# Optimization experiments

Hardware: AMD Instinct MI355X
Metric: run time of the kernel (lower is better)

Reference implementation:

```python
import jax, jax.numpy as jnp
import numpy as np

D, H, W = 64, 128, 128
NUM_LABELS = 2
NUM_ITERS = 5
SIGMA_SPATIAL_BLUR = 1.0   # sigma for the pure spatial Gaussian filter
BLUR_RADIUS = 2            # 5-tap separable kernel
SIGMA_BILAT_SPATIAL = 1.5  # spatial sigma of bilateral filter
SIGMA_BILAT_RANGE = 0.5    # intensity (range) sigma of bilateral filter
LOG_SQRT_2PI = 0.5 * float(np.log(2.0 * np.pi))


def _shift(x, axis, off):
    # zero-padded shift: out[i] = x[i - off] along `axis` (static off)
    if off == 0:
        return x
    pad = [(0, 0)] * x.ndim
    sl = [slice(None)] * x.ndim
    if off > 0:
        pad[axis] = (off, 0)
        sl[axis] = slice(0, x.shape[axis])
    else:
        pad[axis] = (0, -off)
        sl[axis] = slice(-off, x.shape[axis] - off)
    return jnp.pad(x, pad)[tuple(sl)]


def _shift3(x, dz, dy, dx):
    return _shift(_shift(_shift(x, 2, dz), 3, dy), 4, dx)


_offs = np.arange(-BLUR_RADIUS, BLUR_RADIUS + 1)
_k1d = np.exp(-_offs.astype(np.float64) ** 2 / (2.0 * SIGMA_SPATIAL_BLUR ** 2))
_k1d = (_k1d / _k1d.sum()).astype(np.float32)


def _gaussian_blur3d(x):
    # separable normalized Gaussian over the 3 spatial axes (zero padding)
    for ax in (2, 3, 4):
        x = sum(float(_k1d[i]) * _shift(x, ax, int(_offs[i])) for i in range(len(_offs)))
    return x


def _bilateral_weights(image):
    # precompute 27 neighbor weight maps (image is constant across CRF iterations)
    ws, offsets = [], []
    for dz in (-1, 0, 1):
        for dy in (-1, 0, 1):
            for dx in (-1, 0, 1):
                d2 = float(dz * dz + dy * dy + dx * dx)
                img_s = _shift3(image, dz, dy, dx)
                w = jnp.exp(-d2 / (2.0 * SIGMA_BILAT_SPATIAL ** 2)
                            - (image - img_s) ** 2 / (2.0 * SIGMA_BILAT_RANGE ** 2))
                ws.append(w)
                offsets.append((dz, dy, dx))
    den = sum(ws)  # (1,1,D,H,W), broadcasts over labels
    return ws, den, offsets


def _bilateral_apply(q, ws, den, offsets):
    num = sum(w * _shift3(q, dz, dy, dx) for w, (dz, dy, dx) in zip(ws, offsets))
    return num / den


def _crfrnn(image, logits, unary, spatial_w, bilateral_w, compat):
    ws, den, offsets = _bilateral_weights(image)
    cur = logits
    for _ in range(NUM_ITERS):
        qs = jax.nn.softmax(cur, axis=1)                      # (1,L,D,H,W)
        sp = _gaussian_blur3d(qs)                             # spatial message
        bl = _bilateral_apply(qs, ws, den, offsets)           # bilateral message
        msg = (jnp.einsum('lm,bmdhw->bldhw', spatial_w, sp)
               + jnp.einsum('lm,bmdhw->bldhw', bilateral_w, bl))
        pairwise = jnp.einsum('lm,bmdhw->bldhw', compat, msg)
        cur = unary - pairwise
    return jax.nn.softmax(cur, axis=1)


def setup_inputs() -> dict:
    key = jax.random.key(0)
    k1, k2, k3, k4, k5, k6 = jax.random.split(key, 6)
    image = jax.random.normal(k1, (1, 1, D, H, W), dtype=jnp.float32)
    q = jax.random.uniform(k2, (1, 1, D, H, W), dtype=jnp.float32)
    h = jnp.concatenate([1.0 - q, q], axis=1)                 # (1,2,D,H,W)
    f_1 = jax.random.normal(k3, (1, 1, D, H, W), dtype=jnp.float32)
    w_0 = jnp.zeros((1,), dtype=jnp.float32)
    spatial_ker_weights = jax.random.normal(k4, (NUM_LABELS, NUM_LABELS), dtype=jnp.float32)
    bilateral_ker_weights = jax.random.normal(k5, (NUM_LABELS, NUM_LABELS), dtype=jnp.float32)
    compatibility_matrix = jax.random.normal(k6, (NUM_LABELS, NUM_LABELS), dtype=jnp.float32)
    return {'image': image, 'h': h, 'f_1': f_1, 'w_0': w_0,
            'spatial_ker_weights': spatial_ker_weights,
            'bilateral_ker_weights': bilateral_ker_weights,
            'compatibility_matrix': compatibility_matrix}


def reference(image, h, f_1, w_0, spatial_ker_weights, bilateral_ker_weights, compatibility_matrix):
    logits = h
    log_prob = -0.5 * image * image - LOG_SQRT_2PI           # N(0,1).log_prob(image)
    unary = h * (-(w_0[0] + log_prob - f_1))                 # broadcasts (1,1,..) -> (1,2,..)
    h_new = _crfrnn(image, logits, unary, spatial_ker_weights,
                    bilateral_ker_weights, compatibility_matrix)
    return (h_new, f_1)
```

## Files before the change

kernel.cpp:

```cpp
#include <hip/hip_runtime.h>


#define DD 64
#define HH 128
#define WW 128
#define NN (DD*HH*WW)

__device__ __forceinline__ float bfac(int p, int dim) {
    const float K[5] = {0.05448868f, 0.24420134f, 0.40261995f, 0.24420134f, 0.05448868f};
    float s = 0.f;
#pragma unroll
    for (int o = -2; o <= 2; ++o) {
        int pp = p + o;
        s += (pp >= 0 && pp < dim) ? K[o + 2] : 0.f;
    }
    return s;
}

__global__ __launch_bounds__(256) void crf_pre(
    const float* __restrict__ img, const float* __restrict__ h,
    const float* __restrict__ f1, const float* __restrict__ w0,
    const float* __restrict__ sw, const float* __restrict__ bw,
    const float* __restrict__ cm,
    float* __restrict__ dA, float* __restrict__ P)
{
    const float Sc[4] = {1.f, 0.80073740f, 0.64118039f, 0.51341712f};
    int g = blockIdx.x * 256 + threadIdx.x;
    if (g >= NN) return;
    int z = g >> 14, rem = g & 16383, y = rem >> 7, x = rem & 127;

    float cd0 = cm[2] - cm[0], cd1 = cm[3] - cm[1];
    float Ksp = cd0 * sw[0] + cd1 * sw[2];
    float Kbl = cd0 * bw[0] + cd1 * bw[2];

    float Ic = img[g];
    float h0 = h[g], h1 = h[NN + g], fv = f1[g];
    float logp = -0.5f * Ic * Ic - 0.91893853320467274f;
    float t = -(w0[0] + logp - fv);

    float bones = bfac(z, DD) * bfac(y, HH) * bfac(x, WW);

    float den = 0.f, num = 0.f;
#pragma unroll
    for (int dz = -1; dz <= 1; ++dz)
#pragma unroll
        for (int dy = -1; dy <= 1; ++dy)
#pragma unroll
            for (int dx = -1; dx <= 1; ++dx) {
                int nz = z + dz, ny = y + dy, nx = x + dx;
                bool inb = (unsigned)nz < 64u && (unsigned)ny < 128u && (unsigned)nx < 128u;
                float In = inb ? img[g + dz * 16384 + dy * 128 + dx] : 0.f;
                float dd = Ic - In;
                float w = Sc[dz * dz + dy * dy + dx * dx] * __expf(-2.f * dd * dd);
                den += w;
                num += inb ? w : 0.f;
            }
    float Cf = Ksp * bones + Kbl * (num / den);
    dA[g] = h1 - h0;
    P[g]  = (h1 - h0) * t - Cf;
}

template <bool LAST>
__global__ __launch_bounds__(256) void crf_iter(
    const float* __restrict__ dsrc, float* __restrict__ ddst,
    const float* __restrict__ img, const float* __restrict__ P,
    const float* __restrict__ sw, const float* __restrict__ bw,
    const float* __restrict__ cm,
    const float* __restrict__ f1, float* __restrict__ out)
{
    const float K0 = 0.05448868f, K1 = 0.24420134f, K2 = 0.40261995f;
    const float Sc[4] = {1.f, 0.80073740f, 0.64118039f, 0.51341712f};

    __shared__ float qs[12][12][20];
    __shared__ float ims[10][10][20];
    __shared__ float t1[12][12][16];
    __shared__ float t2[12][8][16];

    const int tid = threadIdx.x;
    const int x0 = blockIdx.x * 16, y0 = blockIdx.y * 8, zB = blockIdx.z * 8;

    const float cd0 = cm[2] - cm[0], cd1 = cm[3] - cm[1];
    const float Ac = cd0 * (sw[1] - sw[0]) + cd1 * (sw[3] - sw[2]);
    const float Bc = cd0 * (bw[1] - bw[0]) + cd1 * (bw[3] - bw[2]);

    float* qf = &qs[0][0][0];
    for (int idx = tid; idx < 2880; idx += 256) {
        int lz = idx / 240, r = idx - lz * 240, ly = r / 20, lx = r - ly * 20;
        int gz = zB + lz - 2, gy = y0 + ly - 2, gx = x0 + lx - 2;
        float v = 0.f;
        if ((unsigned)gz < 64u && (unsigned)gy < 128u && (unsigned)gx < 128u)
            v = 1.f / (1.f + __expf(-dsrc[(gz << 14) + (gy << 7) + gx]));
        qf[idx] = v;
    }
    float* imf = &ims[0][0][0];
    for (int idx = tid; idx < 2000; idx += 256) {
        int lz = idx / 200, r = idx - lz * 200, ly = r / 20, lx = r - ly * 20;
        int gz = zB + lz - 1, gy = y0 + ly - 1, gx = x0 + lx - 1;
        float v = 0.f;
        if ((unsigned)gz < 64u && (unsigned)gy < 128u && (unsigned)gx < 128u)
            v = img[(gz << 14) + (gy << 7) + gx];
        imf[idx] = v;
    }
    __syncthreads();

    for (int idx = tid; idx < 576; idx += 256) {
        int lz = idx / 48, r = idx - lz * 48, ly = r / 4, c4 = (r - ly * 4) * 4;
        const float* row = &qs[lz][ly][c4];
        float4 a = *(const float4*)row;
        float4 b = *(const float4*)(row + 4);
        float4 o;
        o.x = K0 * (a.x + b.x) + K1 * (a.y + a.w) + K2 * a.z;
        o.y = K0 * (a.y + b.y) + K1 * (a.z + b.x) + K2 * a.w;
        o.z = K0 * (a.z + b.z) + K1 * (a.w + b.y) + K2 * b.x;
        o.w = K0 * (a.w + b.w) + K1 * (b.x + b.z) + K2 * b.y;
        *(float4*)&t1[lz][ly][c4] = o;
    }
    __syncthreads();

    for (int idx = tid; idx < 384; idx += 256) {
        int lz = idx / 32, r = idx - lz * 32, ly = r / 4, c4 = (r - ly * 4) * 4;
        float4 r0 = *(const float4*)&t1[lz][ly][c4];
        float4 r1 = *(const float4*)&t1[lz][ly + 1][c4];
        float4 r2 = *(const float4*)&t1[lz][ly + 2][c4];
        float4 r3 = *(const float4*)&t1[lz][ly + 3][c4];
        float4 r4 = *(const float4*)&t1[lz][ly + 4][c4];
        float4 o;
        o.x = K0 * (r0.x + r4.x) + K1 * (r1.x + r3.x) + K2 * r2.x;
        o.y = K0 * (r0.y + r4.y) + K1 * (r1.y + r3.y) + K2 * r2.y;
        o.z = K0 * (r0.z + r4.z) + K1 * (r1.z + r3.z) + K2 * r2.z;
        o.w = K0 * (r0.w + r4.w) + K1 * (r1.w + r3.w) + K2 * r2.w;
        *(float4*)&t2[lz][ly][c4] = o;
    }
    __syncthreads();

    const int lx = (tid & 3) * 4;
    const int ly = (tid >> 2) & 7;
    const int lz = tid >> 5;

    float4 za = *(const float4*)&t2[lz][ly][lx];
    float4 zb = *(const float4*)&t2[lz + 1][ly][lx];
    float4 zc = *(const float4*)&t2[lz + 2][ly][lx];
    float4 zd = *(const float4*)&t2[lz + 3][ly][lx];
    float4 ze = *(const float4*)&t2[lz + 4][ly][lx];
    float sp[4];
    sp[0] = K0 * (za.x + ze.x) + K1 * (zb.x + zd.x) + K2 * zc.x;
    sp[1] = K0 * (za.y + ze.y) + K1 * (zb.y + zd.y) + K2 * zc.y;
    sp[2] = K0 * (za.z + ze.z) + K1 * (zb.z + zd.z) + K2 * zc.z;
    sp[3] = K0 * (za.w + ze.w) + K1 * (zb.w + zd.w) + K2 * zc.w;

    float Ic[4];
    {
        float4 c0 = *(const float4*)&ims[lz + 1][ly + 1][lx];
        float4 c1 = *(const float4*)&ims[lz + 1][ly + 1][lx + 4];
        Ic[0] = c0.y; Ic[1] = c0.z; Ic[2] = c0.w; Ic[3] = c1.x;
    }
    float num[4] = {0, 0, 0, 0}, den[4] = {0, 0, 0, 0};
#pragma unroll
    for (int dz = -1; dz <= 1; ++dz) {
#pragma unroll
        for (int dy = -1; dy <= 1; ++dy) {
            float4 qa = *(const float4*)&qs[lz + 2 + dz][ly + 2 + dy][lx];
            float4 qb = *(const float4*)&qs[lz + 2 + dz][ly + 2 + dy][lx + 4];
            float4 ia = *(const float4*)&ims[lz + 1 + dz][ly + 1 + dy][lx];
            float4 ib = *(const float4*)&ims[lz + 1 + dz][ly + 1 + dy][lx + 4];
            float q8[8] = {qa.x, qa.y, qa.z, qa.w, qb.x, qb.y, qb.z, qb.w};
            float i8[8] = {ia.x, ia.y, ia.z, ia.w, ib.x, ib.y, ib.z, ib.w};
#pragma unroll
            for (int dx = -1; dx <= 1; ++dx) {
                const float s = Sc[dz * dz + dy * dy + dx * dx];
#pragma unroll
                for (int xi = 0; xi < 4; ++xi) {
                    float dd = Ic[xi] - i8[1 + xi + dx];
                    float w = s * __expf(-2.f * dd * dd);
                    den[xi] += w;
                    num[xi] += w * q8[2 + xi + dx];
                }
            }
        }
    }

    const int g = ((zB + lz) << 14) + ((y0 + ly) << 7) + (x0 + lx);
    float4 Pv = *(const float4*)&P[g];
    float pr[4] = {Pv.x, Pv.y, Pv.z, Pv.w};
    float dn[4];
#pragma unroll
    for (int xi = 0; xi < 4; ++xi)
        dn[xi] = pr[xi] - Ac * sp[xi] - Bc * (num[xi] / den[xi]);

    if (!LAST) {
        float4 o = {dn[0], dn[1], dn[2], dn[3]};
        *(float4*)&ddst[g] = o;
    } else {
        float q1[4];
#pragma unroll
        for (int xi = 0; xi < 4; ++xi) q1[xi] = 1.f / (1.f + __expf(-dn[xi]));
        float4 o1 = {q1[0], q1[1], q1[2], q1[3]};
        float4 o0 = {1.f - q1[0], 1.f - q1[1], 1.f - q1[2], 1.f - q1[3]};
        *(float4*)&out[g] = o0;
        *(float4*)&out[NN + g] = o1;
        float4 fv = *(const float4*)&f1[g];
        *(float4*)&out[2 * NN + g] = fv;
    }
}

extern "C" void kernel_launch(void* const* d_in, const int* in_sizes, int n_in,
                              void* d_out, int out_size, void* d_ws, size_t ws_size,
                              hipStream_t stream)
{
    const float* img = (const float*)d_in[0];
    const float* h   = (const float*)d_in[1];
    const float* f1  = (const float*)d_in[2];
    const float* w0  = (const float*)d_in[3];
    const float* sw  = (const float*)d_in[4];
    const float* bw  = (const float*)d_in[5];
    const float* cm  = (const float*)d_in[6];
    float* out = (float*)d_out;

    float* dA = (float*)d_ws;
    float* dB = dA + NN;
    float* P  = dB + NN;

    crf_pre<<<NN / 256, 256, 0, stream>>>(img, h, f1, w0, sw, bw, cm, dA, P);

    dim3 grid(WW / 16, HH / 8, DD / 8);
    crf_iter<false><<<grid, 256, 0, stream>>>(dA, dB, img, P, sw, bw, cm, nullptr, nullptr);
    crf_iter<false><<<grid, 256, 0, stream>>>(dB, dA, img, P, sw, bw, cm, nullptr, nullptr);
    crf_iter<false><<<grid, 256, 0, stream>>>(dA, dB, img, P, sw, bw, cm, nullptr, nullptr);
    crf_iter<false><<<grid, 256, 0, stream>>>(dB, dA, img, P, sw, bw, cm, nullptr, nullptr);
    crf_iter<true ><<<grid, 256, 0, stream>>>(dA, nullptr, img, P, sw, bw, cm, f1, out);
}
```

Baseline: 185.6 us.

## Precompute symmetric bilateral weights in fp16 and store softmax probabilities between iterations

The pre-pass now computes the bilateral weights once and stores 13 of the 27 directions as fp16 maps. The other 13 come from symmetry, read at the neighbor's offset, and the center weight is 1. It also precomputes Bc/den per voxel and stores the sigmoid probability, so each iteration skips the 27 exps, the image halo staging and the per-load sigmoid. The cost is much more global memory traffic per iteration (26 fp16 weight loads per voxel, plus M) and some precision loss from fp16 weights. Guard padding zeroed around the weight buffer handles out-of-range symmetric reads.

```diff
diff --git a/kernel.cpp b/kernel.cpp
--- a/kernel.cpp
+++ b/kernel.cpp
@@ -5,6 +5,10 @@
 #define HH 128
 #define WW 128
 #define NN (DD*HH*WW)
+#define GUARD 16520
+
+typedef _Float16 hf;
+typedef _Float16 hf4 __attribute__((ext_vector_type(4)));
 
 __device__ __forceinline__ float bfac(int p, int dim) {
     const float K[5] = {0.05448868f, 0.24420134f, 0.40261995f, 0.24420134f, 0.05448868f};
@@ -22,25 +26,31 @@
     const float* __restrict__ f1, const float* __restrict__ w0,
     const float* __restrict__ sw, const float* __restrict__ bw,
     const float* __restrict__ cm,
-    float* __restrict__ dA, float* __restrict__ P)
+    float* __restrict__ qA, float* __restrict__ P,
+    float* __restrict__ M, hf* __restrict__ W)
 {
     const float Sc[4] = {1.f, 0.80073740f, 0.64118039f, 0.51341712f};
     int g = blockIdx.x * 256 + threadIdx.x;
     if (g >= NN) return;
+    if (g < GUARD) {
+        W[-1 - g] = (hf)0.f;
+        W[13 * NN + g] = (hf)0.f;
+    }
     int z = g >> 14, rem = g & 16383, y = rem >> 7, x = rem & 127;
 
     float cd0 = cm[2] - cm[0], cd1 = cm[3] - cm[1];
     float Ksp = cd0 * sw[0] + cd1 * sw[2];
     float Kbl = cd0 * bw[0] + cd1 * bw[2];
+    float Bc  = cd0 * (bw[1] - bw[0]) + cd1 * (bw[3] - bw[2]);
 
     float Ic = img[g];
     float h0 = h[g], h1 = h[NN + g], fv = f1[g];
     float logp = -0.5f * Ic * Ic - 0.91893853320467274f;
     float t = -(w0[0] + logp - fv);
-
     float bones = bfac(z, DD) * bfac(y, HH) * bfac(x, WW);
 
-    float den = 0.f, num = 0.f;
+    float den = 0.f, numi = 0.f;
+    int o = 0;
 #pragma unroll
     for (int dz = -1; dz <= 1; ++dz)
 #pragma unroll
@@ -53,26 +63,64 @@
                 float dd = Ic - In;
                 float w = Sc[dz * dz + dy * dy + dx * dx] * __expf(-2.f * dd * dd);
                 den += w;
-                num += inb ? w : 0.f;
+                numi += inb ? w : 0.f;
+                if (o >= 14) W[(o - 14) * NN + g] = (hf)w;
+                ++o;
             }
-    float Cf = Ksp * bones + Kbl * (num / den);
-    dA[g] = h1 - h0;
-    P[g]  = (h1 - h0) * t - Cf;
+    float dq = h1 - h0;
+    qA[g] = 1.f / (1.f + __expf(-dq));
+    M[g]  = Bc / den;
+    P[g]  = dq * t - Ksp * bones - Kbl * (numi / den);
+}
+
+__device__ __forceinline__ void ldrow(const float* p, float* r) {
+    float4 a = *(const float4*)p;
+    float4 b = *(const float4*)(p + 4);
+    r[0] = a.x; r[1] = a.y; r[2] = a.z; r[3] = a.w;
+    r[4] = b.x; r[5] = b.y; r[6] = b.z; r[7] = b.w;
+}
+
+template <int OFF, int SH>
+__device__ __forceinline__ void loadw4(const hf* __restrict__ base, int g, float* w) {
+    const hf4* p = (const hf4*)(base + (g + OFF - SH));
+    hf4 a = p[0];
+    if constexpr (SH == 0) {
+        w[0] = (float)a.x; w[1] = (float)a.y; w[2] = (float)a.z; w[3] = (float)a.w;
+    } else {
+        hf4 b = p[1];
+#pragma unroll
+        for (int xi = 0; xi < 4; ++xi) {
+            constexpr int S = SH;
+            int k = S + xi;
+            w[xi] = (k < 4) ? (float)a[k] : (float)b[k - 4];
+        }
+    }
+}
+
+template <int FD, int DZ, int DY, int DX>
+__device__ __forceinline__ void dir_acc(const hf* __restrict__ W, int g,
+                                        const float* rp, const float* rm, float* num) {
+    constexpr int OFF = DZ * 16384 + DY * 128 + DX;
+    constexpr int SB = (((-DX) % 4) + 4) % 4;
+    float wf[4], wb[4];
+    loadw4<0, 0>(W + FD * NN, g, wf);
+    loadw4<-OFF, SB>(W + FD * NN, g, wb);
+#pragma unroll
+    for (int xi = 0; xi < 4; ++xi)
+        num[xi] += wf[xi] * rp[2 + xi + DX] + wb[xi] * rm[2 + xi - DX];
 }
 
 template <bool LAST>
 __global__ __launch_bounds__(256) void crf_iter(
-    const float* __restrict__ dsrc, float* __restrict__ ddst,
-    const float* __restrict__ img, const float* __restrict__ P,
-    const float* __restrict__ sw, const float* __restrict__ bw,
-    const float* __restrict__ cm,
+    const float* __restrict__ qsrc, float* __restrict__ qdst,
+    const float* __restrict__ P, const float* __restrict__ M,
+    const hf* __restrict__ W,
+    const float* __restrict__ sw, const float* __restrict__ cm,
     const float* __restrict__ f1, float* __restrict__ out)
 {
     const float K0 = 0.05448868f, K1 = 0.24420134f, K2 = 0.40261995f;
-    const float Sc[4] = {1.f, 0.80073740f, 0.64118039f, 0.51341712f};
 
     __shared__ float qs[12][12][20];
-    __shared__ float ims[10][10][20];
     __shared__ float t1[12][12][16];
     __shared__ float t2[12][8][16];
 
@@ -81,25 +129,15 @@
 
     const float cd0 = cm[2] - cm[0], cd1 = cm[3] - cm[1];
     const float Ac = cd0 * (sw[1] - sw[0]) + cd1 * (sw[3] - sw[2]);
-    const float Bc = cd0 * (bw[1] - bw[0]) + cd1 * (bw[3] - bw[2]);
 
     float* qf = &qs[0][0][0];
     for (int idx = tid; idx < 2880; idx += 256) {
-        int lz = idx / 240, r = idx - lz * 240, ly = r / 20, lx = r - ly * 20;
-        int gz = zB + lz - 2, gy = y0 + ly - 2, gx = x0 + lx - 2;
+        int lz = idx / 240, r = idx - lz * 240, ly = r / 20, lx2 = r - ly * 20;
+        int gz = zB + lz - 2, gy = y0 + ly - 2, gx = x0 + lx2 - 2;
         float v = 0.f;
         if ((unsigned)gz < 64u && (unsigned)gy < 128u && (unsigned)gx < 128u)
-            v = 1.f / (1.f + __expf(-dsrc[(gz << 14) + (gy << 7) + gx]));
+            v = qsrc[(gz << 14) + (gy << 7) + gx];
         qf[idx] = v;
-    }
-    float* imf = &ims[0][0][0];
-    for (int idx = tid; idx < 2000; idx += 256) {
-        int lz = idx / 200, r = idx - lz * 200, ly = r / 20, lx = r - ly * 20;
-        int gz = zB + lz - 1, gy = y0 + ly - 1, gx = x0 + lx - 1;
-        float v = 0.f;
-        if ((unsigned)gz < 64u && (unsigned)gy < 128u && (unsigned)gx < 128u)
-            v = img[(gz << 14) + (gy << 7) + gx];
-        imf[idx] = v;
     }
     __syncthreads();
 
@@ -148,54 +186,57 @@
     sp[2] = K0 * (za.z + ze.z) + K1 * (zb.z + zd.z) + K2 * zc.z;
     sp[3] = K0 * (za.w + ze.w) + K1 * (zb.w + zd.w) + K2 * zc.w;
 
-    float Ic[4];
-    {
-        float4 c0 = *(const float4*)&ims[lz + 1][ly + 1][lx];
-        float4 c1 = *(const float4*)&ims[lz + 1][ly + 1][lx + 4];
-        Ic[0] = c0.y; Ic[1] = c0.z; Ic[2] = c0.w; Ic[3] = c1.x;
-    }
-    float num[4] = {0, 0, 0, 0}, den[4] = {0, 0, 0, 0};
-#pragma unroll
-    for (int dz = -1; dz <= 1; ++dz) {
-#pragma unroll
-        for (int dy = -1; dy <= 1; ++dy) {
-            float4 qa = *(const float4*)&qs[lz + 2 + dz][ly + 2 + dy][lx];
-            float4 qb = *(const float4*)&qs[lz + 2 + dz][ly + 2 + dy][lx + 4];
-            float4 ia = *(const float4*)&ims[lz + 1 + dz][ly + 1 + dy][lx];
-            float4 ib = *(const float4*)&ims[lz + 1 + dz][ly + 1 + dy][lx + 4];
-            float q8[8] = {qa.x, qa.y, qa.z, qa.w, qb.x, qb.y, qb.z, qb.w};
-            float i8[8] = {ia.x, ia.y, ia.z, ia.w, ib.x, ib.y, ib.z, ib.w};
-#pragma unroll
-            for (int dx = -1; dx <= 1; ++dx) {
-                const float s = Sc[dz * dz + dy * dy + dx * dx];
-#pragma unroll
-                for (int xi = 0; xi < 4; ++xi) {
-                    float dd = Ic[xi] - i8[1 + xi + dx];
-                    float w = s * __expf(-2.f * dd * dd);
-                    den[xi] += w;
-                    num[xi] += w * q8[2 + xi + dx];
-                }
-            }
-        }
-    }
-
     const int g = ((zB + lz) << 14) + ((y0 + ly) << 7) + (x0 + lx);
+
+    float num[4];
+    float rc[8], rp[8], rm[8];
+    ldrow(&qs[lz + 2][ly + 2][lx], rc);
+#pragma unroll
+    for (int xi = 0; xi < 4; ++xi) num[xi] = rc[2 + xi];
+
+    dir_acc<0, 0, 0, 1>(W, g, rc, rc, num);
+
+    ldrow(&qs[lz + 2][ly + 3][lx], rp);
+    ldrow(&qs[lz + 2][ly + 1][lx], rm);
+    dir_acc<1, 0, 1, -1>(W, g, rp, rm, num);
+    dir_acc<2, 0, 1, 0>(W, g, rp, rm, num);
+    dir_acc<3, 0, 1, 1>(W, g, rp, rm, num);
+
+    ldrow(&qs[lz + 3][ly + 1][lx], rp);
+    ldrow(&qs[lz + 1][ly + 3][lx], rm);
+    dir_acc<4, 1, -1, -1>(W, g, rp, rm, num);
+    dir_acc<5, 1, -1, 0>(W, g, rp, rm, num);
+    dir_acc<6, 1, -1, 1>(W, g, rp, rm, num);
+
+    ldrow(&qs[lz + 3][ly + 2][lx], rp);
+    ldrow(&qs[lz + 1][ly + 2][lx], rm);
+    dir_acc<7, 1, 0, -1>(W, g, rp, rm, num);
+    dir_acc<8, 1, 0, 0>(W, g, rp, rm, num);
+    dir_acc<9, 1, 0, 1>(W, g, rp, rm, num);
+
+    ldrow(&qs[lz + 3][ly + 3][lx], rp);
+    ldrow(&qs[lz + 1][ly + 1][lx], rm);
+    dir_acc<10, 1, 1, -1>(W, g, rp, rm, num);
+    dir_acc<11, 1, 1, 0>(W, g, rp, rm, num);
+    dir_acc<12, 1, 1, 1>(W, g, rp, rm, num);
+
     float4 Pv = *(const float4*)&P[g];
+    float4 Mv = *(const float4*)&M[g];
     float pr[4] = {Pv.x, Pv.y, Pv.z, Pv.w};
-    float dn[4];
-#pragma unroll
-    for (int xi = 0; xi < 4; ++xi)
-        dn[xi] = pr[xi] - Ac * sp[xi] - Bc * (num[xi] / den[xi]);
+    float mv[4] = {Mv.x, Mv.y, Mv.z, Mv.w};
+    float qn[4];
+#pragma unroll
+    for (int xi = 0; xi < 4; ++xi) {
+        float dn = pr[xi] - Ac * sp[xi] - mv[xi] * num[xi];
+        qn[xi] = 1.f / (1.f + __expf(-dn));
+    }
 
     if (!LAST) {
-        float4 o = {dn[0], dn[1], dn[2], dn[3]};
-        *(float4*)&ddst[g] = o;
+        float4 o = {qn[0], qn[1], qn[2], qn[3]};
+        *(float4*)&qdst[g] = o;
     } else {
-        float q1[4];
-#pragma unroll
-        for (int xi = 0; xi < 4; ++xi) q1[xi] = 1.f / (1.f + __expf(-dn[xi]));
-        float4 o1 = {q1[0], q1[1], q1[2], q1[3]};
-        float4 o0 = {1.f - q1[0], 1.f - q1[1], 1.f - q1[2], 1.f - q1[3]};
+        float4 o1 = {qn[0], qn[1], qn[2], qn[3]};
+        float4 o0 = {1.f - qn[0], 1.f - qn[1], 1.f - qn[2], 1.f - qn[3]};
         *(float4*)&out[g] = o0;
         *(float4*)&out[NN + g] = o1;
         float4 fv = *(const float4*)&f1[g];
@@ -216,16 +257,18 @@
     const float* cm  = (const float*)d_in[6];
     float* out = (float*)d_out;
 
-    float* dA = (float*)d_ws;
-    float* dB = dA + NN;
-    float* P  = dB + NN;
-
-    crf_pre<<<NN / 256, 256, 0, stream>>>(img, h, f1, w0, sw, bw, cm, dA, P);
+    float* qA = (float*)d_ws;
+    float* qB = qA + NN;
+    float* P  = qB + NN;
+    float* M  = P + NN;
+    hf* W = (hf*)(M + NN) + GUARD;
+
+    crf_pre<<<NN / 256, 256, 0, stream>>>(img, h, f1, w0, sw, bw, cm, qA, P, M, W);
 
     dim3 grid(WW / 16, HH / 8, DD / 8);
-    crf_iter<false><<<grid, 256, 0, stream>>>(dA, dB, img, P, sw, bw, cm, nullptr, nullptr);
-    crf_iter<false><<<grid, 256, 0, stream>>>(dB, dA, img, P, sw, bw, cm, nullptr, nullptr);
-    crf_iter<false><<<grid, 256, 0, stream>>>(dA, dB, img, P, sw, bw, cm, nullptr, nullptr);
-    crf_iter<false><<<grid, 256, 0, stream>>>(dB, dA, img, P, sw, bw, cm, nullptr, nullptr);
-    crf_iter<true ><<<grid, 256, 0, stream>>>(dA, nullptr, img, P, sw, bw, cm, f1, out);
-}
+    crf_iter<false><<<grid, 256, 0, stream>>>(qA, qB, P, M, W, sw, cm, nullptr, nullptr);
+    crf_iter<false><<<grid, 256, 0, stream>>>(qB, qA, P, M, W, sw, cm, nullptr, nullptr);
+    crf_iter<false><<<grid, 256, 0, stream>>>(qA, qB, P, M, W, sw, cm, nullptr, nullptr);
+    crf_iter<false><<<grid, 256, 0, stream>>>(qB, qA, P, M, W, sw, cm, nullptr, nullptr);
+    crf_iter<true ><<<grid, 256, 0, stream>>>(qA, nullptr, P, M, W, sw, cm, f1, out);
+}
```

New measurement: 269.2 us. 1.45x slower.
